# Kernel tuning notes

Hardware: AMD Instinct MI355X
Metric: run time of the kernel (lower is better)

The kernel has to match this reference:

```python
import jax, jax.numpy as jnp
import numpy as np

N_HEAD, D_HEAD, D_MODEL = 8, 64, 512
MEM_LEN, QLEN, BSZ = 1024, 1024, 4
KLEN = MEM_LEN + QLEN
CONV_PAD = 3  # conv_size // 2 for conv_size = 7
LN_EPS = 1e-5


def setup_inputs() -> dict:
    key = jax.random.key(0)
    ks = jax.random.split(key, 16)
    s = 0.02
    inp = {
        "w": jax.random.normal(ks[0], (QLEN, BSZ, D_MODEL), jnp.float32),
        "r": jax.random.normal(ks[1], (KLEN, D_MODEL), jnp.float32),
        "mems": jax.random.normal(ks[2], (MEM_LEN, BSZ, D_MODEL), jnp.float32),
        "r_w_bias": jax.random.normal(ks[3], (N_HEAD, D_HEAD), jnp.float32) * s,
        "r_r_bias": jax.random.normal(ks[4], (N_HEAD, D_HEAD), jnp.float32) * s,
        "qkv_W": jax.random.normal(ks[5], (3 * N_HEAD * D_HEAD, D_MODEL), jnp.float32) * s,
        "r_W": jax.random.normal(ks[6], (N_HEAD * D_HEAD, D_MODEL), jnp.float32) * s,
        "conv_q_w": jax.random.normal(ks[7], (D_HEAD, D_HEAD, 7), jnp.float32) * 0.05,
        "conv_q_b": jnp.zeros((D_HEAD,), jnp.float32),
        "conv_k_w": jax.random.normal(ks[8], (D_HEAD, D_HEAD, 7), jnp.float32) * 0.05,
        "conv_k_b": jnp.zeros((D_HEAD,), jnp.float32),
        "conv_v_w": jax.random.normal(ks[9], (D_HEAD, D_HEAD, 7), jnp.float32) * 0.05,
        "conv_v_b": jnp.zeros((D_HEAD,), jnp.float32),
        "o_W": jax.random.normal(ks[10], (D_MODEL, N_HEAD * D_HEAD), jnp.float32) * s,
        "ln_g": jnp.ones((D_MODEL,), jnp.float32),
        "ln_b": jnp.zeros((D_MODEL,), jnp.float32),
        # causal-with-memory mask: query i may attend keys j <= i + MEM_LEN
        "attn_mask": jnp.arange(KLEN)[None, :] > (jnp.arange(QLEN)[:, None] + MEM_LEN),
    }
    return inp


def _conv1d(x, wt, b):
    # x: [N, C, L], wt: [O, I, K], same padding (pad=3)
    y = jax.lax.conv_general_dilated(x, wt, (1,), [(CONV_PAD, CONV_PAD)],
                                     dimension_numbers=("NCH", "OIH", "NCH"))
    return y + b[None, :, None]


def _head_conv(x, wt, b, length, bsz):
    # x: [len, b, H*Dh] -> per-head Conv1d over time -> [len, b, H, Dh]
    xh = x.reshape(length, bsz, N_HEAD, D_HEAD).transpose(2, 1, 3, 0)  # [H,b,Dh,len]
    xh = xh.reshape(N_HEAD * bsz, D_HEAD, length)
    xh = _conv1d(xh, wt, b)
    return xh.reshape(N_HEAD, bsz, D_HEAD, length).transpose(3, 1, 0, 2)  # [len,b,H,Dh]


def _rel_shift(x):
    # x: [qlen, rlen, b, n]
    q, rl, b, n = x.shape
    zp = jnp.zeros((q, 1, b, n), x.dtype)
    xp = jnp.concatenate([zp, x], axis=1).reshape(rl + 1, q, b, n)[1:]
    return xp.reshape(q, rl, b, n)


def _layer_norm(x, g, b):
    mu = jnp.mean(x, axis=-1, keepdims=True)
    var = jnp.mean(jnp.square(x - mu), axis=-1, keepdims=True)
    return (x - mu) * jax.lax.rsqrt(var + LN_EPS) * g + b


def reference(w, r, mems, r_w_bias, r_r_bias, qkv_W, r_W,
              conv_q_w, conv_q_b, conv_k_w, conv_k_b, conv_v_w, conv_v_b,
              o_W, ln_g, ln_b, attn_mask):
    qlen, bsz = w.shape[0], w.shape[1]
    cat = jnp.concatenate([mems, w], axis=0)           # [klen, b, d_model]
    klen = cat.shape[0]
    w_heads = cat @ qkv_W.T                            # [klen, b, 3*H*Dh]
    r_head_k = (r @ r_W.T).reshape(klen, N_HEAD, D_HEAD)
    q, k, v = jnp.split(w_heads, 3, axis=-1)
    q = q[-qlen:]
    # per-head conv augmentation of Q/K/V
    q = _head_conv(q, conv_q_w, conv_q_b, qlen, bsz)   # [qlen,b,H,Dh]
    k = _head_conv(k, conv_k_w, conv_k_b, klen, bsz)   # [klen,b,H,Dh]
    v = _head_conv(v, conv_v_w, conv_v_b, klen, bsz)
    scale = 1.0 / (D_HEAD ** 0.5)
    AC = jnp.einsum("ibnd,jbnd->ijbn", q + r_w_bias, k)
    BD = jnp.einsum("ibnd,jnd->ijbn", q + r_r_bias, r_head_k)
    BD = _rel_shift(BD)
    attn_score = (AC + BD) * scale                     # [qlen,klen,b,H]
    attn_score = jnp.where(attn_mask[:, :, None, None], -jnp.inf, attn_score)
    attn_prob = jax.nn.softmax(attn_score, axis=1)
    attn_vec = jnp.einsum("ijbn,jbnd->ibnd", attn_prob, v)
    attn_vec = attn_vec.reshape(qlen, bsz, N_HEAD * D_HEAD)
    attn_out = attn_vec @ o_W.T                        # [qlen,b,d_model]
    return _layer_norm(w + attn_out, ln_g, ln_b)
```

## Files before the change

kernel.cpp:

```cpp
#include <hip/hip_runtime.h>
#include <hip/hip_bf16.h>

typedef unsigned short u16;
typedef unsigned int   u32;
typedef u16 u16x8 __attribute__((ext_vector_type(8)));
typedef u16 u16x4 __attribute__((ext_vector_type(4)));
typedef float f32x4 __attribute__((ext_vector_type(4)));
typedef short s16x8 __attribute__((ext_vector_type(8)));
typedef u32 u32x4 __attribute__((ext_vector_type(4)));

__device__ __forceinline__ float b2f(u16 u) { return __uint_as_float(((u32)u) << 16); }
__device__ __forceinline__ u16 f2b(float f) {
  u32 u = __float_as_uint(f);
  u32 r = u + 0x7FFFu + ((u >> 16) & 1u);
  return (u16)(r >> 16);
}
__device__ __forceinline__ u32 f2b2(float lo, float hi) {
  __hip_bfloat162 h = __float22bfloat162_rn(make_float2(lo, hi));
  union { __hip_bfloat162 h; u32 u; } cv;
  cv.h = h;
  return cv.u;
}

#define MFMA_B16(A, B, C) __builtin_amdgcn_mfma_f32_16x16x32_bf16((A), (B), (C), 0, 0, 0)

__device__ __forceinline__ void gl16(const u16* g, u16* l) {
  __builtin_amdgcn_global_load_lds(
      (const __attribute__((address_space(1))) void*)g,
      (__attribute__((address_space(3))) void*)l, 16, 0, 0);
}

__global__ __launch_bounds__(256) void cvt_all(
    const float* __restrict__ mems, const float* __restrict__ w,
    const float* __restrict__ r, const float* __restrict__ qkvW,
    const float* __restrict__ rW, const float* __restrict__ oW,
    const float* __restrict__ cqw, const float* __restrict__ ckw,
    const float* __restrict__ cvw,
    u16* __restrict__ catb, u16* __restrict__ rb, u16* __restrict__ qkvWb,
    u16* __restrict__ rWb, u16* __restrict__ oWb, u16* __restrict__ cwb) {
  if (blockIdx.x >= 3200) {
    int idx = (blockIdx.x - 3200) * 256 + threadIdx.x;
    if (idx >= 86016) return;
    int wsel = idx / 28672, rem = idx % 28672;
    const float* src = (wsel == 0) ? cqw : ((wsel == 1) ? ckw : cvw);
    int s = rem / 4096, r2 = rem % 4096;
    int d = r2 / 64, eswz = r2 % 64;
    int e = (((eswz >> 3) ^ (d & 7)) << 3) + (eswz & 7);
    cwb[idx] = f2b(src[d * 448 + e * 7 + s]);
    return;
  }
  long g = ((long)blockIdx.x * 256 + threadIdx.x) * 8;
  const float* src;
  u16* dst;
  if (g < 4194304) {
    src = (g < 2097152) ? (mems + g) : (w + (g - 2097152));
    dst = catb + g;
  } else if (g < 5242880) {
    src = r + (g - 4194304);    dst = rb + (g - 4194304);
  } else if (g < 6029312) {
    src = qkvW + (g - 5242880); dst = qkvWb + (g - 5242880);
  } else if (g < 6291456) {
    src = rW + (g - 6029312);   dst = rWb + (g - 6029312);
  } else {
    src = oW + (g - 6291456);   dst = oWb + (g - 6291456);
  }
  f32x4 a = *(const f32x4*)src;
  f32x4 b = *(const f32x4*)(src + 4);
  u32x4 p = (u32x4){f2b2(a[0], a[1]), f2b2(a[2], a[3]),
                    f2b2(b[0], b[1]), f2b2(b[2], b[3])};
  *(u32x4*)dst = p;
}

__global__ __launch_bounds__(256) void gemm_fused(
    const u16* __restrict__ catb, const u16* __restrict__ qkvWb,
    u16* __restrict__ Wh, const u16* __restrict__ rb,
    const u16* __restrict__ rWb, u16* __restrict__ Rk) {
  int bx = blockIdx.x, by = blockIdx.y;
  const u16 *A, *B;
  u16* C;
  int N;
  if (bx < 12) {
    if (bx < 4 && by < 32) return;
    A = catb; B = qkvWb; C = Wh; N = 1536;
  } else {
    if (by >= 16) return;
    A = rb; B = rWb; C = Rk; N = 512; bx = 0;
  }
  const int K = 512;
  __shared__ u16 A_s[128 * 32];
  __shared__ u16 B_s[128 * 32];
  int tid = threadIdx.x;
  int wave = tid >> 6, lane = tid & 63, quad = lane >> 4, l16 = lane & 15;
  int wr = wave >> 1, wc = wave & 1;

  f32x4 acc[4][4];
#pragma unroll
  for (int a = 0; a < 4; a++)
#pragma unroll
    for (int bb = 0; bb < 4; bb++) acc[a][bb] = (f32x4){0.f, 0.f, 0.f, 0.f};

  const u16* Ab = A + (size_t)by * 128 * K;
  const u16* Bb = B + (size_t)bx * 128 * K;
  int lrow = lane >> 2;
  int lkc  = (lane & 3) * 8;
  int L0 = wave * 2;

  for (int k0 = 0; k0 < K; k0 += 32) {
    __syncthreads();
#pragma unroll
    for (int m = 0; m < 2; m++) {
      int L = L0 + m;
      int row = L * 16 + lrow;
      gl16(Ab + (size_t)row * K + k0 + lkc, &A_s[L * 512 + lane * 8]);
      gl16(Bb + (size_t)row * K + k0 + lkc, &B_s[L * 512 + lane * 8]);
    }
    __syncthreads();

    s16x8 af[4], bf[4];
#pragma unroll
    for (int a = 0; a < 4; a++)
      af[a] = *(const s16x8*)&A_s[(wr * 64 + a * 16 + l16) * 32 + quad * 8];
#pragma unroll
    for (int bb = 0; bb < 4; bb++)
      bf[bb] = *(const s16x8*)&B_s[(wc * 64 + bb * 16 + l16) * 32 + quad * 8];
#pragma unroll
    for (int a = 0; a < 4; a++)
#pragma unroll
      for (int bb = 0; bb < 4; bb++)
        acc[a][bb] = MFMA_B16(af[a], bf[bb], acc[a][bb]);
  }

#pragma unroll
  for (int a = 0; a < 4; a++)
#pragma unroll
    for (int bb = 0; bb < 4; bb++) {
      int row = by * 128 + wr * 64 + a * 16 + quad * 4;
      int col = bx * 128 + wc * 64 + bb * 16 + l16;
#pragma unroll
      for (int reg = 0; reg < 4; reg++)
        C[(size_t)(row + reg) * N + col] = f2b(acc[a][bb][reg]);
    }
}

__global__ __launch_bounds__(256) void gemm_mfma(
    const u16* __restrict__ A, const u16* __restrict__ B,
    u16* __restrict__ C, int N, int K) {
  __shared__ u16 A_s[128 * 32];
  __shared__ u16 B_s[128 * 32];
  int tid = threadIdx.x;
  int bx = blockIdx.x, by = blockIdx.y;
  int wave = tid >> 6, lane = tid & 63, quad = lane >> 4, l16 = lane & 15;
  int wr = wave >> 1, wc = wave & 1;

  f32x4 acc[4][4];
#pragma unroll
  for (int a = 0; a < 4; a++)
#pragma unroll
    for (int bb = 0; bb < 4; bb++) acc[a][bb] = (f32x4){0.f, 0.f, 0.f, 0.f};

  const u16* Ab = A + (size_t)by * 128 * K;
  const u16* Bb = B + (size_t)bx * 128 * K;
  int lrow = lane >> 2;
  int lkc  = (lane & 3) * 8;
  int L0 = wave * 2;

  for (int k0 = 0; k0 < K; k0 += 32) {
    __syncthreads();
#pragma unroll
    for (int m = 0; m < 2; m++) {
      int L = L0 + m;
      int row = L * 16 + lrow;
      gl16(Ab + (size_t)row * K + k0 + lkc, &A_s[L * 512 + lane * 8]);
      gl16(Bb + (size_t)row * K + k0 + lkc, &B_s[L * 512 + lane * 8]);
    }
    __syncthreads();

    s16x8 af[4], bf[4];
#pragma unroll
    for (int a = 0; a < 4; a++)
      af[a] = *(const s16x8*)&A_s[(wr * 64 + a * 16 + l16) * 32 + quad * 8];
#pragma unroll
    for (int bb = 0; bb < 4; bb++)
      bf[bb] = *(const s16x8*)&B_s[(wc * 64 + bb * 16 + l16) * 32 + quad * 8];
#pragma unroll
    for (int a = 0; a < 4; a++)
#pragma unroll
      for (int bb = 0; bb < 4; bb++)
        acc[a][bb] = MFMA_B16(af[a], bf[bb], acc[a][bb]);
  }

#pragma unroll
  for (int a = 0; a < 4; a++)
#pragma unroll
    for (int bb = 0; bb < 4; bb++) {
      int row = by * 128 + wr * 64 + a * 16 + quad * 4;
      int col = bx * 128 + wc * 64 + bb * 16 + l16;
#pragma unroll
      for (int reg = 0; reg < 4; reg++)
        C[(size_t)(row + reg) * N + col] = f2b(acc[a][bb][reg]);
    }
}

__global__ __launch_bounds__(256) void conv_fused(
    const u16* __restrict__ Wh, const u16* __restrict__ cwb,
    const float* __restrict__ cqb, const float* __restrict__ ckb,
    const float* __restrict__ cvb,
    u16* __restrict__ qpost, u16* __restrict__ kpost, u16* __restrict__ vpostT) {
  __shared__ u16 wT_s[7 * 4096];
  __shared__ u16 in_s[134 * 64];
  int blk = blockIdx.x;
  int part, lt0, len, tshift, vt;
  const float* cbp;
  const u16* cwp;
  u16* outp;
  if (blk < 2) {
    part = 0; lt0 = blk * 4; len = 1024; tshift = 1024; vt = 0;
    cbp = cqb; cwp = cwb; outp = qpost;
  } else if (blk < 6) {
    part = 1; lt0 = (blk - 2) * 4; len = 2048; tshift = 0; vt = 0;
    cbp = ckb; cwp = cwb + 28672; outp = kpost;
  } else {
    part = 2; lt0 = (blk - 6) * 4; len = 2048; tshift = 0; vt = 1;
    cbp = cvb; cwp = cwb + 57344; outp = vpostT;
  }
  int tid = threadIdx.x;
  int b = blockIdx.y, n = blockIdx.z;
  int wave = tid >> 6, lane = tid & 63, quad = lane >> 4, l16 = lane & 15;

  for (int idx = tid * 8; idx < 28672; idx += 2048)
    *(u16x8*)&wT_s[idx] = *(const u16x8*)(cwp + idx);

  float bias[4];
#pragma unroll
  for (int nn = 0; nn < 4; nn++) bias[nn] = cbp[nn * 16 + l16];

  int e8 = tid & 7;
  int colb = part * 512 + n * 64 + e8 * 8;

  for (int ch = 0; ch < 4; ch++) {
    int t0 = (lt0 + ch) * 128;
    if (ch) __syncthreads();
    for (int r = tid >> 3; r < 134; r += 32) {
      int tt = t0 + r - 3;
      u16x8 v = {0, 0, 0, 0, 0, 0, 0, 0};
      if (tt >= 0 && tt < len)
        v = *(const u16x8*)(Wh + (size_t)((tt + tshift) * 4 + b) * 1536 + colb);
      *(u16x8*)&in_s[r * 64 + ((e8 ^ (r & 7)) << 3)] = v;
    }
    __syncthreads();

    f32x4 acc[2][4];
#pragma unroll
    for (int mt = 0; mt < 2; mt++)
#pragma unroll
      for (int nn = 0; nn < 4; nn++) acc[mt][nn] = (f32x4){0.f, 0.f, 0.f, 0.f};

#pragma unroll
    for (int s = 0; s < 7; s++) {
#pragma unroll
      for (int ks = 0; ks < 2; ks++) {
        int eb = ks * 4 + quad;
        s16x8 af[2];
#pragma unroll
        for (int mt = 0; mt < 2; mt++) {
          int r = wave * 32 + mt * 16 + l16 + s;
          af[mt] = *(const s16x8*)&in_s[r * 64 + ((eb ^ (r & 7)) << 3)];
        }
#pragma unroll
        for (int nn = 0; nn < 4; nn++) {
          int d = nn * 16 + l16;
          s16x8 bf = *(const s16x8*)&wT_s[s * 4096 + d * 64 + ((eb ^ (d & 7)) << 3)];
          acc[0][nn] = MFMA_B16(af[0], bf, acc[0][nn]);
          acc[1][nn] = MFMA_B16(af[1], bf, acc[1][nn]);
        }
      }
    }

    if (!vt) {
#pragma unroll
      for (int mt = 0; mt < 2; mt++)
#pragma unroll
        for (int nn = 0; nn < 4; nn++) {
          int col = nn * 16 + l16;
#pragma unroll
          for (int reg = 0; reg < 4; reg++) {
            int t = t0 + wave * 32 + mt * 16 + quad * 4 + reg;
            outp[(size_t)((t * 4 + b) * 8 + n) * 64 + col] = f2b(acc[mt][nn][reg] + bias[nn]);
          }
        }
    } else {
      __syncthreads();
      u16* T = in_s;
#pragma unroll
      for (int mt = 0; mt < 2; mt++)
#pragma unroll
        for (int nn = 0; nn < 4; nn++) {
          union { u32 u[2]; u16x4 v; } pk;
          pk.u[0] = f2b2(acc[mt][nn][0] + bias[nn], acc[mt][nn][1] + bias[nn]);
          pk.u[1] = f2b2(acc[mt][nn][2] + bias[nn], acc[mt][nn][3] + bias[nn]);
          *(u16x4*)&T[(nn * 16 + l16) * 132 + wave * 32 + mt * 16 + quad * 4] = pk.v;
        }
      __syncthreads();
      int dS = tid >> 2, tq = tid & 3;
      u16* gdst = outp + ((size_t)(b * 8 + n) * 64 + dS) * 2048 + t0 + tq * 32;
      const u16* tsrc = &T[dS * 132 + tq * 32];
#pragma unroll
      for (int c = 0; c < 4; c++)
        *(u16x8*)(gdst + c * 8) = *(const u16x8*)(tsrc + c * 8);
    }
  }
}

__global__ __launch_bounds__(256) void attn_mfma(
    const u16* __restrict__ qpost, const u16* __restrict__ kpost,
    const u16* __restrict__ vpostT, const u16* __restrict__ Rk,
    const float* __restrict__ rwb, const float* __restrict__ rrb,
    u16* __restrict__ av_out) {
  __shared__ u16 K_s[64 * 64];
  __shared__ u16 V_s[64 * 64];
  __shared__ u16 R_s[128 * 64];
  __shared__ u16 BD_s[4][80 * 20];
  __shared__ u16 P_s[4][16 * 64];
  int tid = threadIdx.x;
  int bxr = blockIdx.x;
  int it = (bxr & 1) ? (15 - (bxr >> 1)) : (bxr >> 1);
  int i0 = it * 64, b = blockIdx.y, n = blockIdx.z;
  int wave = tid >> 6, lane = tid & 63, quad = lane >> 4, l16 = lane & 15;
  int i0w = i0 + wave * 16;
  int rbaseW = 48 - wave * 16;
  int rbase = 960 - i0;
  int ntiles = it + 17;
  const float SC = 0.125f * 1.44269504f;

  s16x8 aw[2], ar[2];
  {
    int ig = i0w + l16;
    const u16* qp = qpost + ((size_t)((ig * 4 + b) * 8 + n)) * 64;
#pragma unroll
    for (int ks = 0; ks < 2; ks++) {
      int d0 = ks * 32 + quad * 8;
      u16x8 qv = *(const u16x8*)(qp + d0);
      union { u32x4 u; s16x8 s; } pw, pr;
#pragma unroll
      for (int e2 = 0; e2 < 4; e2++) {
        float qa = b2f(qv[2 * e2]), qb = b2f(qv[2 * e2 + 1]);
        pw.u[e2] = f2b2(qa + rwb[n * 64 + d0 + 2 * e2], qb + rwb[n * 64 + d0 + 2 * e2 + 1]);
        pr.u[e2] = f2b2(qa + rrb[n * 64 + d0 + 2 * e2], qb + rrb[n * 64 + d0 + 2 * e2 + 1]);
      }
      aw[ks] = pw.s;
      ar[ks] = pr.s;
    }
  }

  {
    int rrI = tid >> 1, h = tid & 1;
    int g = rbase + rrI;
    int prow = g & 127;
    const u16* rp2 = Rk + (size_t)g * 512 + n * 64 + h * 32;
#pragma unroll
    for (int c = 0; c < 4; c++) {
      int kb = h * 4 + c;
      *(u16x8*)&R_s[prow * 64 + ((kb ^ (prow & 7)) << 3)] = *(const u16x8*)(rp2 + c * 8);
    }
  }

  f32x4 O[4];
#pragma unroll
  for (int c = 0; c < 4; c++) O[c] = (f32x4){0.f, 0.f, 0.f, 0.f};
  float l4[4] = {0.f, 0.f, 0.f, 0.f};

  int jl = tid >> 2, q4 = tid & 3;
  u16x8 kv0, kv1, vv0, vv1, rv0, rv1;
  {
    size_t src = ((size_t)(jl * 4 + b) * 8 + n) * 64 + q4 * 16;
    kv0 = *(const u16x8*)(kpost + src);
    kv1 = *(const u16x8*)(kpost + src + 8);
    const u16* vsrc = vpostT + ((size_t)(b * 8 + n) * 64 + jl) * 2048 + q4 * 16;
    vv0 = *(const u16x8*)(vsrc);
    vv1 = *(const u16x8*)(vsrc + 8);
  }
  {
    int g = rbase + 128 + jl;
    rv0 = (u16x8){0, 0, 0, 0, 0, 0, 0, 0};
    rv1 = rv0;
    if (g < 2048) {
      const u16* rp2 = Rk + (size_t)g * 512 + n * 64 + q4 * 16;
      rv0 = *(const u16x8*)(rp2);
      rv1 = *(const u16x8*)(rp2 + 8);
    }
  }

  for (int t = 0; t < ntiles; t++) {
    int j0 = t * 64;
    __syncthreads();
    *(u16x8*)&K_s[jl * 64 + (((2 * q4) ^ (jl & 7)) << 3)] = kv0;
    *(u16x8*)&K_s[jl * 64 + (((2 * q4 + 1) ^ (jl & 7)) << 3)] = kv1;
    *(u16x8*)&V_s[jl * 64 + (((2 * q4) ^ (jl & 7)) << 3)] = vv0;
    *(u16x8*)&V_s[jl * 64 + (((2 * q4 + 1) ^ (jl & 7)) << 3)] = vv1;
    if (t > 0) {
      int g = rbase + j0 + 64 + jl;
      int prow = g & 127;
      *(u16x8*)&R_s[prow * 64 + (((2 * q4) ^ (prow & 7)) << 3)] = rv0;
      *(u16x8*)&R_s[prow * 64 + (((2 * q4 + 1) ^ (prow & 7)) << 3)] = rv1;
    }
    __syncthreads();

    if (t + 1 < ntiles) {
      int j0n = j0 + 64;
      size_t src = ((size_t)((j0n + jl) * 4 + b) * 8 + n) * 64 + q4 * 16;
      kv0 = *(const u16x8*)(kpost + src);
      kv1 = *(const u16x8*)(kpost + src + 8);
      const u16* vsrc = vpostT + ((size_t)(b * 8 + n) * 64 + jl) * 2048 + j0n + q4 * 16;
      vv0 = *(const u16x8*)(vsrc);
      vv1 = *(const u16x8*)(vsrc + 8);
      int g = rbase + j0n + 64 + jl;
      rv0 = (u16x8){0, 0, 0, 0, 0, 0, 0, 0};
      rv1 = rv0;
      if (g < 2048) {
        const u16* rp2 = Rk + (size_t)g * 512 + n * 64 + q4 * 16;
        rv0 = *(const u16x8*)(rp2);
        rv1 = *(const u16x8*)(rp2 + 8);
      }
    }

    f32x4 sc4[4];
#pragma unroll
    for (int c = 0; c < 4; c++) {
      f32x4 tt = (f32x4){0.f, 0.f, 0.f, 0.f};
#pragma unroll
      for (int ks = 0; ks < 2; ks++) {
        int j = c * 16 + l16;
        int kb = ks * 4 + quad;
        s16x8 kf = *(const s16x8*)&K_s[j * 64 + ((kb ^ (j & 7)) << 3)];
        tt = MFMA_B16(aw[ks], kf, tt);
      }
      sc4[c] = tt;
    }
    int rbj = rbase + j0 + rbaseW;
#pragma unroll
    for (int cb = 0; cb < 5; cb++) {
      f32x4 tt = (f32x4){0.f, 0.f, 0.f, 0.f};
#pragma unroll
      for (int ks = 0; ks < 2; ks++) {
        int prow = (rbj + cb * 16 + l16) & 127;
        int kb = ks * 4 + quad;
        s16x8 rf = *(const s16x8*)&R_s[prow * 64 + ((kb ^ (prow & 7)) << 3)];
        tt = MFMA_B16(ar[ks], rf, tt);
      }
      union { u32 u[2]; u16x4 v; } pk;
      pk.u[0] = f2b2(tt[0], tt[1]);
      pk.u[1] = f2b2(tt[2], tt[3]);
      *(u16x4*)&BD_s[wave][(cb * 16 + l16) * 20 + quad * 4] = pk.v;
    }

#pragma unroll
    for (int c = 0; c < 4; c++)
#pragma unroll
      for (int reg = 0; reg < 4; reg++) {
        int iw = quad * 4 + reg;
        int uw = c * 16 + l16 + 15 - iw;
        float bd = b2f(BD_s[wave][uw * 20 + iw]);
        float val = (sc4[c][reg] + bd) * SC;
        int jg = j0 + c * 16 + l16;
        float p = (jg > i0w + iw + 1024) ? 0.f : __builtin_amdgcn_exp2f(val);
        l4[reg] += p;
        int jb = c * 2 + (l16 >> 3);
        P_s[wave][iw * 64 + ((jb ^ (iw & 7)) << 3) + (l16 & 7)] = f2b(p);
      }

#pragma unroll
    for (int cd = 0; cd < 4; cd++) {
      int d = cd * 16 + l16;
#pragma unroll
      for (int ks = 0; ks < 2; ks++) {
        int kb = ks * 4 + quad;
        s16x8 pf = *(const s16x8*)&P_s[wave][l16 * 64 + ((kb ^ (l16 & 7)) << 3)];
        s16x8 vf = *(const s16x8*)&V_s[d * 64 + ((kb ^ (d & 7)) << 3)];
        O[cd] = MFMA_B16(pf, vf, O[cd]);
      }
    }
  }

#pragma unroll
  for (int off = 1; off < 16; off <<= 1)
#pragma unroll
    for (int reg = 0; reg < 4; reg++) l4[reg] += __shfl_xor(l4[reg], off);

#pragma unroll
  for (int reg = 0; reg < 4; reg++) {
    float inv = 1.0f / l4[reg];
    int ig2 = i0w + quad * 4 + reg;
#pragma unroll
    for (int cd = 0; cd < 4; cd++)
      av_out[((size_t)(ig2 * 4 + b)) * 512 + n * 64 + cd * 16 + l16] =
          f2b(O[cd][reg] * inv);
  }
}

__global__ __launch_bounds__(64) void lnorm(
    const float* __restrict__ w, const u16* __restrict__ ao,
    const float* __restrict__ g, const float* __restrict__ bb,
    float* __restrict__ out) {
  int row = blockIdx.x, t = threadIdx.x;
  const float* wp = w + (size_t)row * 512 + t * 8;
  const u16* ap = ao + (size_t)row * 512 + t * 8;
  f32x4 w0 = *(const f32x4*)wp;
  f32x4 w1 = *(const f32x4*)(wp + 4);
  u16x8 av = *(const u16x8*)ap;
  float x[8];
  float sum = 0.f;
#pragma unroll
  for (int e = 0; e < 4; e++) {
    x[e] = w0[e] + b2f(av[e]);
    x[4 + e] = w1[e] + b2f(av[4 + e]);
  }
#pragma unroll
  for (int e = 0; e < 8; e++) sum += x[e];
#pragma unroll
  for (int off = 1; off < 64; off <<= 1) sum += __shfl_xor(sum, off);
  float mu = sum * (1.0f / 512.0f);
  float vs = 0.f;
#pragma unroll
  for (int e = 0; e < 8; e++) {
    float d = x[e] - mu;
    vs += d * d;
  }
#pragma unroll
  for (int off = 1; off < 64; off <<= 1) vs += __shfl_xor(vs, off);
  float rs = rsqrtf(vs * (1.0f / 512.0f) + 1e-5f);
  f32x4 g0 = *(const f32x4*)(g + t * 8);
  f32x4 g1 = *(const f32x4*)(g + t * 8 + 4);
  f32x4 b0 = *(const f32x4*)(bb + t * 8);
  f32x4 b1 = *(const f32x4*)(bb + t * 8 + 4);
  f32x4 o0, o1;
#pragma unroll
  for (int e = 0; e < 4; e++) {
    o0[e] = (x[e] - mu) * rs * g0[e] + b0[e];
    o1[e] = (x[4 + e] - mu) * rs * g1[e] + b1[e];
  }
  float* op = out + (size_t)row * 512 + t * 8;
  *(f32x4*)op = o0;
  *(f32x4*)(op + 4) = o1;
}

extern "C" void kernel_launch(void* const* d_in, const int* in_sizes, int n_in,
                              void* d_out, int out_size, void* d_ws, size_t ws_size,
                              hipStream_t stream) {
  (void)in_sizes; (void)n_in; (void)out_size;
  const float* w    = (const float*)d_in[0];
  const float* r    = (const float*)d_in[1];
  const float* mems = (const float*)d_in[2];
  const float* rwb  = (const float*)d_in[3];
  const float* rrb  = (const float*)d_in[4];
  const float* qkvW = (const float*)d_in[5];
  const float* rW   = (const float*)d_in[6];
  const float* cqw  = (const float*)d_in[7];
  const float* cqb  = (const float*)d_in[8];
  const float* ckw  = (const float*)d_in[9];
  const float* ckb  = (const float*)d_in[10];
  const float* cvw  = (const float*)d_in[11];
  const float* cvb  = (const float*)d_in[12];
  const float* oW   = (const float*)d_in[13];
  const float* lng  = (const float*)d_in[14];
  const float* lnb  = (const float*)d_in[15];

  u16* ws     = (u16*)d_ws;
  u16* Wh     = ws;
  u16* qpost  = Wh + 12582912;
  u16* kpost  = qpost + 2097152;
  u16* vpostT = kpost + 4194304;
  u16* Rk     = vpostT + 4194304;
  u16* av     = Rk + 1048576;
  u16* aout   = av + 2097152;
  u16* qkvWb  = aout + 2097152;
  u16* rWb    = qkvWb + 786432;
  u16* oWb    = rWb + 262144;
  u16* cwb    = oWb + 262144;
  u16* catb   = av;
  u16* rb     = qpost;
  if (ws_size < 59416576ull) return;

  cvt_all<<<3536, 256, 0, stream>>>(mems, w, r, qkvW, rW, oW, cqw, ckw, cvw,
                                    catb, rb, qkvWb, rWb, oWb, cwb);
  gemm_fused<<<dim3(13, 64), 256, 0, stream>>>(catb, qkvWb, Wh, rb, rWb, Rk);
  conv_fused<<<dim3(10, 4, 8), 256, 0, stream>>>(Wh, cwb, cqb, ckb, cvb, qpost, kpost, vpostT);
  attn_mfma<<<dim3(16, 4, 8), 256, 0, stream>>>(qpost, kpost, vpostT, Rk, rwb, rrb, av);
  gemm_mfma<<<dim3(4, 32), 256, 0, stream>>>(av, oWb, aout, 512, 512);
  lnorm<<<4096, 64, 0, stream>>>(w, aout, lng, lnb, (float*)d_out);
}
```

Measured before the change: 235.1 us.

## Double-buffer GEMM LDS tiles, skip mask on interior attention tiles, pack lnorm rows

Both GEMM kernels now keep two LDS buffers per operand and prefetch the next K-slice while running MFMAs on the current one, so each iteration needs one barrier instead of two. The attention softmax applies the causal mask comparison only on the last key tile, and the P fragments are loaded once and reused across the output columns. The layer-norm kernel now handles four rows per 256-thread block instead of one row per 64-thread block. The double buffering doubles LDS use per GEMM block, which may lower occupancy.

```diff
diff --git a/kernel.cpp b/kernel.cpp
--- a/kernel.cpp
+++ b/kernel.cpp
@@ -87,8 +87,8 @@
     A = rb; B = rWb; C = Rk; N = 512; bx = 0;
   }
   const int K = 512;
-  __shared__ u16 A_s[128 * 32];
-  __shared__ u16 B_s[128 * 32];
+  __shared__ u16 A_s[2][128 * 32];
+  __shared__ u16 B_s[2][128 * 32];
   int tid = threadIdx.x;
   int wave = tid >> 6, lane = tid & 63, quad = lane >> 4, l16 = lane & 15;
   int wr = wave >> 1, wc = wave & 1;
@@ -105,29 +105,41 @@
   int lkc  = (lane & 3) * 8;
   int L0 = wave * 2;
 
+#pragma unroll
+  for (int m = 0; m < 2; m++) {
+    int L = L0 + m, row = L * 16 + lrow;
+    gl16(Ab + (size_t)row * K + lkc, &A_s[0][L * 512 + lane * 8]);
+    gl16(Bb + (size_t)row * K + lkc, &B_s[0][L * 512 + lane * 8]);
+  }
+  __syncthreads();
+
+  int cur = 0;
   for (int k0 = 0; k0 < K; k0 += 32) {
-    __syncthreads();
-#pragma unroll
-    for (int m = 0; m < 2; m++) {
-      int L = L0 + m;
-      int row = L * 16 + lrow;
-      gl16(Ab + (size_t)row * K + k0 + lkc, &A_s[L * 512 + lane * 8]);
-      gl16(Bb + (size_t)row * K + k0 + lkc, &B_s[L * 512 + lane * 8]);
-    }
-    __syncthreads();
+    int kn = k0 + 32;
+    if (kn < K) {
+#pragma unroll
+      for (int m = 0; m < 2; m++) {
+        int L = L0 + m, row = L * 16 + lrow;
+        gl16(Ab + (size_t)row * K + kn + lkc, &A_s[cur ^ 1][L * 512 + lane * 8]);
+        gl16(Bb + (size_t)row * K + kn + lkc, &B_s[cur ^ 1][L * 512 + lane * 8]);
+      }
+    }
 
     s16x8 af[4], bf[4];
 #pragma unroll
     for (int a = 0; a < 4; a++)
-      af[a] = *(const s16x8*)&A_s[(wr * 64 + a * 16 + l16) * 32 + quad * 8];
+      af[a] = *(const s16x8*)&A_s[cur][(wr * 64 + a * 16 + l16) * 32 + quad * 8];
 #pragma unroll
     for (int bb = 0; bb < 4; bb++)
-      bf[bb] = *(const s16x8*)&B_s[(wc * 64 + bb * 16 + l16) * 32 + quad * 8];
+      bf[bb] = *(const s16x8*)&B_s[cur][(wc * 64 + bb * 16 + l16) * 32 + quad * 8];
 #pragma unroll
     for (int a = 0; a < 4; a++)
 #pragma unroll
       for (int bb = 0; bb < 4; bb++)
         acc[a][bb] = MFMA_B16(af[a], bf[bb], acc[a][bb]);
+
+    __syncthreads();
+    cur ^= 1;
   }
 
 #pragma unroll
@@ -145,8 +157,8 @@
 __global__ __launch_bounds__(256) void gemm_mfma(
     const u16* __restrict__ A, const u16* __restrict__ B,
     u16* __restrict__ C, int N, int K) {
-  __shared__ u16 A_s[128 * 32];
-  __shared__ u16 B_s[128 * 32];
+  __shared__ u16 A_s[2][128 * 32];
+  __shared__ u16 B_s[2][128 * 32];
   int tid = threadIdx.x;
   int bx = blockIdx.x, by = blockIdx.y;
   int wave = tid >> 6, lane = tid & 63, quad = lane >> 4, l16 = lane & 15;
@@ -164,29 +176,41 @@
   int lkc  = (lane & 3) * 8;
   int L0 = wave * 2;
 
+#pragma unroll
+  for (int m = 0; m < 2; m++) {
+    int L = L0 + m, row = L * 16 + lrow;
+    gl16(Ab + (size_t)row * K + lkc, &A_s[0][L * 512 + lane * 8]);
+    gl16(Bb + (size_t)row * K + lkc, &B_s[0][L * 512 + lane * 8]);
+  }
+  __syncthreads();
+
+  int cur = 0;
   for (int k0 = 0; k0 < K; k0 += 32) {
-    __syncthreads();
-#pragma unroll
-    for (int m = 0; m < 2; m++) {
-      int L = L0 + m;
-      int row = L * 16 + lrow;
-      gl16(Ab + (size_t)row * K + k0 + lkc, &A_s[L * 512 + lane * 8]);
-      gl16(Bb + (size_t)row * K + k0 + lkc, &B_s[L * 512 + lane * 8]);
-    }
-    __syncthreads();
+    int kn = k0 + 32;
+    if (kn < K) {
+#pragma unroll
+      for (int m = 0; m < 2; m++) {
+        int L = L0 + m, row = L * 16 + lrow;
+        gl16(Ab + (size_t)row * K + kn + lkc, &A_s[cur ^ 1][L * 512 + lane * 8]);
+        gl16(Bb + (size_t)row * K + kn + lkc, &B_s[cur ^ 1][L * 512 + lane * 8]);
+      }
+    }
 
     s16x8 af[4], bf[4];
 #pragma unroll
     for (int a = 0; a < 4; a++)
-      af[a] = *(const s16x8*)&A_s[(wr * 64 + a * 16 + l16) * 32 + quad * 8];
+      af[a] = *(const s16x8*)&A_s[cur][(wr * 64 + a * 16 + l16) * 32 + quad * 8];
 #pragma unroll
     for (int bb = 0; bb < 4; bb++)
-      bf[bb] = *(const s16x8*)&B_s[(wc * 64 + bb * 16 + l16) * 32 + quad * 8];
+      bf[bb] = *(const s16x8*)&B_s[cur][(wc * 64 + bb * 16 + l16) * 32 + quad * 8];
 #pragma unroll
     for (int a = 0; a < 4; a++)
 #pragma unroll
       for (int bb = 0; bb < 4; bb++)
         acc[a][bb] = MFMA_B16(af[a], bf[bb], acc[a][bb]);
+
+    __syncthreads();
+    cur ^= 1;
   }
 
 #pragma unroll
@@ -311,6 +335,25 @@
   }
 }
 
+#define SOFTMAX_BLOCK(MASKED)                                                  \
+  _Pragma("unroll")                                                            \
+  for (int c = 0; c < 4; c++)                                                  \
+    _Pragma("unroll")                                                          \
+    for (int reg = 0; reg < 4; reg++) {                                        \
+      int iw = quad * 4 + reg;                                                 \
+      int uw = c * 16 + l16 + 15 - iw;                                         \
+      float bd = b2f(BD_s[wave][uw * 20 + iw]);                                \
+      float val = (sc4[c][reg] + bd) * SC;                                     \
+      float p = __builtin_amdgcn_exp2f(val);                                   \
+      if (MASKED) {                                                            \
+        int jg = j0 + c * 16 + l16;                                            \
+        if (jg > i0w + iw + 1024) p = 0.f;                                     \
+      }                                                                        \
+      l4[reg] += p;                                                            \
+      int jb = c * 2 + (l16 >> 3);                                             \
+      P_s[wave][iw * 64 + ((jb ^ (iw & 7)) << 3) + (l16 & 7)] = f2b(p);        \
+    }
+
 __global__ __launch_bounds__(256) void attn_mfma(
     const u16* __restrict__ qpost, const u16* __restrict__ kpost,
     const u16* __restrict__ vpostT, const u16* __restrict__ Rk,
@@ -453,30 +496,26 @@
       *(u16x4*)&BD_s[wave][(cb * 16 + l16) * 20 + quad * 4] = pk.v;
     }
 
-#pragma unroll
-    for (int c = 0; c < 4; c++)
-#pragma unroll
-      for (int reg = 0; reg < 4; reg++) {
-        int iw = quad * 4 + reg;
-        int uw = c * 16 + l16 + 15 - iw;
-        float bd = b2f(BD_s[wave][uw * 20 + iw]);
-        float val = (sc4[c][reg] + bd) * SC;
-        int jg = j0 + c * 16 + l16;
-        float p = (jg > i0w + iw + 1024) ? 0.f : __builtin_amdgcn_exp2f(val);
-        l4[reg] += p;
-        int jb = c * 2 + (l16 >> 3);
-        P_s[wave][iw * 64 + ((jb ^ (iw & 7)) << 3) + (l16 & 7)] = f2b(p);
-      }
-
+    if (t + 1 < ntiles) {
+      SOFTMAX_BLOCK(0)
+    } else {
+      SOFTMAX_BLOCK(1)
+    }
+
+    s16x8 pf[2];
+#pragma unroll
+    for (int ks = 0; ks < 2; ks++) {
+      int kb = ks * 4 + quad;
+      pf[ks] = *(const s16x8*)&P_s[wave][l16 * 64 + ((kb ^ (l16 & 7)) << 3)];
+    }
 #pragma unroll
     for (int cd = 0; cd < 4; cd++) {
       int d = cd * 16 + l16;
 #pragma unroll
       for (int ks = 0; ks < 2; ks++) {
         int kb = ks * 4 + quad;
-        s16x8 pf = *(const s16x8*)&P_s[wave][l16 * 64 + ((kb ^ (l16 & 7)) << 3)];
         s16x8 vf = *(const s16x8*)&V_s[d * 64 + ((kb ^ (d & 7)) << 3)];
-        O[cd] = MFMA_B16(pf, vf, O[cd]);
+        O[cd] = MFMA_B16(pf[ks], vf, O[cd]);
       }
     }
   }
@@ -497,11 +536,12 @@
   }
 }
 
-__global__ __launch_bounds__(64) void lnorm(
+__global__ __launch_bounds__(256) void lnorm(
     const float* __restrict__ w, const u16* __restrict__ ao,
     const float* __restrict__ g, const float* __restrict__ bb,
     float* __restrict__ out) {
-  int row = blockIdx.x, t = threadIdx.x;
+  int row = blockIdx.x * 4 + (threadIdx.x >> 6);
+  int t = threadIdx.x & 63;
   const float* wp = w + (size_t)row * 512 + t * 8;
   const u16* ap = ao + (size_t)row * 512 + t * 8;
   f32x4 w0 = *(const f32x4*)wp;
@@ -586,5 +626,5 @@
   conv_fused<<<dim3(10, 4, 8), 256, 0, stream>>>(Wh, cwb, cqb, ckb, cvb, qpost, kpost, vpostT);
   attn_mfma<<<dim3(16, 4, 8), 256, 0, stream>>>(qpost, kpost, vpostT, Rk, rwb, rrb, av);
   gemm_mfma<<<dim3(4, 32), 256, 0, stream>>>(av, oWb, aout, 512, 512);
-  lnorm<<<4096, 64, 0, stream>>>(w, aout, lng, lnb, (float*)d_out);
-}
+  lnorm<<<1024, 256, 0, stream>>>(w, aout, lng, lnb, (float*)d_out);
+}
```

After: 239.8 us. About the same (+2.0%).
